# Kernel optimization log

Measured on AMD Instinct MI355X. Metric: run time of the kernel, lower is better.

## Reference

```python
import jax, jax.numpy as jnp
import numpy as np

N_NODES = 10000
DEG = 32
N_EDGES = N_NODES * DEG
IN_FEATS = 256
HEADS = 8
OUT_FEATS = 64
NEG_SLOPE = 0.2


def setup_inputs() -> dict:
    key = jax.random.key(0)
    k1, k2, k3, k4, k5 = jax.random.split(key, 5)
    feat = jax.random.normal(k1, (N_NODES, IN_FEATS), dtype=jnp.float32)
    # fc weight [in_feats, heads*out_feats] (applied as feat @ W)
    W = jax.random.normal(k2, (IN_FEATS, HEADS * OUT_FEATS), dtype=jnp.float32) * (1.0 / np.sqrt(IN_FEATS))
    attn_l = jax.random.normal(k3, (HEADS, OUT_FEATS), dtype=jnp.float32) * 0.1
    attn_r = jax.random.normal(k4, (HEADS, OUT_FEATS), dtype=jnp.float32) * 0.1
    # every node gets DEG incoming edges -> no zero in-degree (softmax well-defined)
    dst = jnp.repeat(jnp.arange(N_NODES, dtype=jnp.int32), DEG)
    src = jax.random.randint(k5, (N_EDGES,), 0, N_NODES, dtype=jnp.int32)
    return {"feat": feat, "W": W, "attn_l": attn_l, "attn_r": attn_r, "src": src, "dst": dst}


def reference(feat, W, attn_l, attn_r, src, dst):
    N = feat.shape[0]
    H, D = attn_l.shape
    # linear projection: [N, H, D]
    ft = (feat @ W).reshape(N, H, D)
    # per-node additive attention logits: [N, H]
    el = jnp.einsum('nhd,hd->nh', ft, attn_l)
    er = jnp.einsum('nhd,hd->nh', ft, attn_r)
    # edge logits (u_add_v) + LeakyReLU: [E, H]
    e = el[src] + er[dst]
    e = jnp.where(e > 0, e, NEG_SLOPE * e)
    # edge softmax segmented by destination node
    m = jax.ops.segment_max(e, dst, num_segments=N)          # [N, H]
    ex = jnp.exp(e - m[dst])                                  # [E, H]
    denom = jax.ops.segment_sum(ex, dst, num_segments=N)     # [N, H]
    a = ex / denom[dst]                                       # [E, H]
    # weighted aggregation (u_mul_e -> sum): [N, H, D]
    rst = jax.ops.segment_sum(ft[src] * a[:, :, None], dst, num_segments=N)
    # module returns attention with trailing singleton dim ([E, H, 1])
    return rst, a[:, :, None]
```

## Files before the change

kernel.cpp:

```cpp
#include <hip/hip_runtime.h>

#define N_NODES   10000
#define M_PAD     10112
#define DEG       32
#define IN_FEATS  256
#define HEADS     8
#define OUT_FEATS 64
#define HD        512
#define NEG_SLOPE 0.2f

typedef short bf16x8 __attribute__((ext_vector_type(8)));
typedef float f32x4  __attribute__((ext_vector_type(4)));

__device__ __forceinline__ ushort f2bf(float x) {
    union { float f; unsigned u; } c; c.f = x;
    unsigned r = (c.u + 0x7fffu + ((c.u >> 16) & 1u)) >> 16;
    return (ushort)r;
}
__device__ __forceinline__ float bfbits2f(unsigned hi_bits) {
    union { unsigned u; float f; } c; c.u = hi_bits;
    return c.f;
}

__global__ __launch_bounds__(256) void convert_all(const float* __restrict__ f,
                                                   ushort* __restrict__ fb,
                                                   const float* __restrict__ W,
                                                   ushort* __restrict__ Bt) {
    __shared__ ushort s[64][72];
    const int b = blockIdx.x;
    const int t = threadIdx.x;
    if (b < 2500) {
        const int i = b * 256 + t;
        const float4 v = reinterpret_cast<const float4*>(f)[i];
        ushort4 o;
        o.x = f2bf(v.x); o.y = f2bf(v.y); o.z = f2bf(v.z); o.w = f2bf(v.w);
        reinterpret_cast<ushort4*>(fb)[i] = o;
        return;
    }
    const int bb = b - 2500;
    const int kb = (bb & 3) * 64;
    const int nb = (bb >> 2) * 64;
    #pragma unroll
    for (int rep = 0; rep < 4; ++rep) {
        const int kk = rep * 16 + (t >> 4);
        const int nn = (t & 15) * 4;
        const float4 v = *reinterpret_cast<const float4*>(&W[(size_t)(kb + kk) * HD + nb + nn]);
        s[nn + 0][kk] = f2bf(v.x);
        s[nn + 1][kk] = f2bf(v.y);
        s[nn + 2][kk] = f2bf(v.z);
        s[nn + 3][kk] = f2bf(v.w);
    }
    __syncthreads();
    const int nn = t >> 2;
    const int k0 = (t & 3) * 16;
    #pragma unroll
    for (int c = 0; c < 2; ++c) {
        *reinterpret_cast<uint4*>(&Bt[(size_t)(nb + nn) * IN_FEATS + kb + k0 + c * 8]) =
            *reinterpret_cast<const uint4*>(&s[nn][k0 + c * 8]);
    }
}

__global__ __launch_bounds__(256) void gemm_logits(const ushort* __restrict__ A,
                                                   const ushort* __restrict__ Bt,
                                                   const float* __restrict__ attn_l,
                                                   const float* __restrict__ attn_r,
                                                   ushort* __restrict__ C,
                                                   float* __restrict__ el,
                                                   float* __restrict__ er) {
    __shared__ ushort As[128 * 32];
    __shared__ ushort Bs[128 * 32];
    const int t    = threadIdx.x;
    const int lane = t & 63;
    const int m0   = blockIdx.x * 128;
    const int n0   = blockIdx.y * 128;
    const int wave = t >> 6;
    const int wr   = (wave >> 1) * 64;
    const int wc   = (wave & 1) * 64;

    const int srow0 = t >> 2;
    const int srow1 = 64 + (t >> 2);
    const int sq    = t & 3;
    const int sq0   = sq ^ ((srow0 >> 1) & 3);
    const int sq1   = sq ^ ((srow1 >> 1) & 3);

    uint4 ra0, ra1, rb0, rb1;
#define LOADREGS(K0)                                                                   \
    do {                                                                               \
        ra0 = *reinterpret_cast<const uint4*>(A  + (size_t)(m0 + srow0) * IN_FEATS + (K0) + sq * 8); \
        ra1 = *reinterpret_cast<const uint4*>(A  + (size_t)(m0 + srow1) * IN_FEATS + (K0) + sq * 8); \
        rb0 = *reinterpret_cast<const uint4*>(Bt + (size_t)(n0 + srow0) * IN_FEATS + (K0) + sq * 8); \
        rb1 = *reinterpret_cast<const uint4*>(Bt + (size_t)(n0 + srow1) * IN_FEATS + (K0) + sq * 8); \
    } while (0)

    f32x4 acc[4][4];
    #pragma unroll
    for (int i = 0; i < 4; ++i)
        #pragma unroll
        for (int j = 0; j < 4; ++j)
            acc[i][j] = (f32x4){0.f, 0.f, 0.f, 0.f};

    const int rqoff = (((lane >> 4) ^ (((lane & 15) >> 1) & 3)) * 8);
    const int rl    = lane & 15;

    LOADREGS(0);
    for (int k0 = 0; k0 < IN_FEATS; k0 += 32) {
        __syncthreads();
        *reinterpret_cast<uint4*>(As + srow0 * 32 + sq0 * 8) = ra0;
        *reinterpret_cast<uint4*>(As + srow1 * 32 + sq1 * 8) = ra1;
        *reinterpret_cast<uint4*>(Bs + srow0 * 32 + sq0 * 8) = rb0;
        *reinterpret_cast<uint4*>(Bs + srow1 * 32 + sq1 * 8) = rb1;
        __syncthreads();
        if (k0 + 32 < IN_FEATS) LOADREGS(k0 + 32);

        bf16x8 af[4], bfr[4];
        #pragma unroll
        for (int i = 0; i < 4; ++i)
            af[i] = *reinterpret_cast<const bf16x8*>(As + (wr + i * 16 + rl) * 32 + rqoff);
        #pragma unroll
        for (int j = 0; j < 4; ++j)
            bfr[j] = *reinterpret_cast<const bf16x8*>(Bs + (wc + j * 16 + rl) * 32 + rqoff);
        #pragma unroll
        for (int i = 0; i < 4; ++i)
            #pragma unroll
            for (int j = 0; j < 4; ++j)
                acc[i][j] = __builtin_amdgcn_mfma_f32_16x16x32_bf16(af[i], bfr[j], acc[i][j], 0, 0, 0);
    }
#undef LOADREGS

    const int g    = lane >> 4;
    const int hblk = (n0 + wc) >> 6;
    float al[4], ar[4];
    #pragma unroll
    for (int j = 0; j < 4; ++j) {
        al[j] = attn_l[hblk * OUT_FEATS + j * 16 + rl];
        ar[j] = attn_r[hblk * OUT_FEATS + j * 16 + rl];
    }

    #pragma unroll
    for (int i = 0; i < 4; ++i) {
        #pragma unroll
        for (int r = 0; r < 4; ++r) {
            const int gm = m0 + wr + i * 16 + g * 4 + r;
            ushort* dst = C + (size_t)gm * HD + n0 + wc + rl;
            float sl = 0.f, sr = 0.f;
            #pragma unroll
            for (int j = 0; j < 4; ++j) {
                dst[j * 16] = f2bf(acc[i][j][r]);
                sl = fmaf(acc[i][j][r], al[j], sl);
                sr = fmaf(acc[i][j][r], ar[j], sr);
            }
            sl += __shfl_xor(sl, 1, 64); sr += __shfl_xor(sr, 1, 64);
            sl += __shfl_xor(sl, 2, 64); sr += __shfl_xor(sr, 2, 64);
            sl += __shfl_xor(sl, 4, 64); sr += __shfl_xor(sr, 4, 64);
            sl += __shfl_xor(sl, 8, 64); sr += __shfl_xor(sr, 8, 64);
            if (rl == 0 && gm < N_NODES) {
                el[gm * HEADS + hblk] = sl;
                er[gm * HEADS + hblk] = sr;
            }
        }
    }
}

__global__ __launch_bounds__(256) void softmax_kernel(const float* __restrict__ el,
                                                      const float* __restrict__ er,
                                                      const int* __restrict__ src,
                                                      float* __restrict__ out_a) {
    __shared__ int   s_src[DEG];
    __shared__ float s_a[DEG][HEADS];

    const int n = blockIdx.x;
    const int t = threadIdx.x;

    if (t < DEG) s_src[t] = src[n * DEG + t];
    __syncthreads();

    const int h = t >> 5;
    const int j = t & 31;
    const int s = s_src[j];
    float e = el[s * HEADS + h] + er[n * HEADS + h];
    e = (e > 0.f) ? e : NEG_SLOPE * e;

    float m = e;
    #pragma unroll
    for (int msk = 16; msk; msk >>= 1) m = fmaxf(m, __shfl_xor(m, msk, 64));
    const float ex = __expf(e - m);
    float sum = ex;
    #pragma unroll
    for (int msk = 16; msk; msk >>= 1) sum += __shfl_xor(sum, msk, 64);
    s_a[j][h] = ex / sum;
    __syncthreads();

    out_a[(size_t)n * 256 + t] = s_a[t >> 3][t & 7];
}

__global__ __launch_bounds__(256) void agg_static(const uint* __restrict__ ftb_dw,
                                                  const float* __restrict__ el,
                                                  const float* __restrict__ er,
                                                  const int* __restrict__ src,
                                                  float* __restrict__ rst) {
    __shared__ int   s_src[8][DEG];
    __shared__ float s_a[8][DEG];

    const int b = blockIdx.x;
    const int s = b & 7;
    const int c = b >> 3;
    const int t = threadIdx.x;
    const int w  = t >> 6;
    const int l  = t & 63;
    const int hi = l >> 5;
    const int li = l & 31;
    const int wn = 2 * w + hi;

    s_src[t >> 5][t & 31] = src[c * 256 + t];

    const int n     = c * 8 + wn;
    const int dwcol = s * 32 + li;

    uint uv[DEG];
    #pragma unroll
    for (int j = 0; j < DEG; ++j)
        uv[j] = ftb_dw[(size_t)s_src[wn][j] * 256 + dwcol];

    float e = el[s_src[wn][li] * HEADS + s] + er[n * HEADS + s];
    e = (e > 0.f) ? e : NEG_SLOPE * e;
    float m = e;
    #pragma unroll
    for (int msk = 16; msk; msk >>= 1) m = fmaxf(m, __shfl_xor(m, msk, 64));
    const float ex = __expf(e - m);
    float sum = ex;
    #pragma unroll
    for (int msk = 16; msk; msk >>= 1) sum += __shfl_xor(sum, msk, 64);
    s_a[wn][li] = ex / sum;

    float a0 = 0.f, a1 = 0.f;
    #pragma unroll
    for (int j = 0; j < DEG; ++j) {
        const float wt = s_a[wn][j];
        a0 = fmaf(wt, bfbits2f(uv[j] << 16), a0);
        a1 = fmaf(wt, bfbits2f(uv[j] & 0xffff0000u), a1);
    }
    *reinterpret_cast<float2*>(&rst[(size_t)n * HD + s * 64 + 2 * li]) = make_float2(a0, a1);
}

extern "C" void kernel_launch(void* const* d_in, const int* in_sizes, int n_in,
                              void* d_out, int out_size, void* d_ws, size_t ws_size,
                              hipStream_t stream) {
    const float* feat   = (const float*)d_in[0];
    const float* W      = (const float*)d_in[1];
    const float* attn_l = (const float*)d_in[2];
    const float* attn_r = (const float*)d_in[3];
    const int*   src    = (const int*)d_in[4];

    float* out_rst = (float*)d_out;
    float* out_a   = out_rst + (size_t)N_NODES * HD;

    char* w = (char*)d_ws;
    ushort* feat_bf = (ushort*)w;  w += (size_t)M_PAD * IN_FEATS * 2;
    ushort* W_bt    = (ushort*)w;  w += (size_t)HD * IN_FEATS * 2;
    ushort* ftb     = (ushort*)w;  w += (size_t)M_PAD * HD * 2;
    float*  el      = (float*)w;   w += (size_t)N_NODES * HEADS * 4;
    float*  er      = (float*)w;   w += (size_t)N_NODES * HEADS * 4;

    convert_all<<<2532, 256, 0, stream>>>(feat, feat_bf, W, W_bt);
    gemm_logits<<<dim3(M_PAD / 128, HD / 128), 256, 0, stream>>>(feat_bf, W_bt, attn_l, attn_r,
                                                                 ftb, el, er);
    softmax_kernel<<<N_NODES, 256, 0, stream>>>(el, er, src, out_a);
    agg_static<<<N_NODES / 8 * 8, 256, 0, stream>>>((const uint*)ftb, el, er, src, out_rst);
}
```

Measured before the change: 60.97 us.

## Fuse feat bf16 conversion into GEMM loads and reuse softmax weights in aggregation

The GEMM now reads fp32 features directly, converts them to bf16 in registers before staging to LDS, and guards out-of-range rows. This removes the separate feature conversion pass and its intermediate buffer. The softmax kernel also writes a head-major copy of the attention weights, which the aggregation kernel loads instead of recomputing logits, max and exp. The trade-off is double the A-operand global traffic in the GEMM, plus an extra 10 MB write and read of attention weights.

Result: slower. 79.81 us (+30.9%).

```diff
diff --git a/kernel.cpp b/kernel.cpp
--- a/kernel.cpp
+++ b/kernel.cpp
@@ -17,29 +17,21 @@
     unsigned r = (c.u + 0x7fffu + ((c.u >> 16) & 1u)) >> 16;
     return (ushort)r;
 }
+__device__ __forceinline__ uint pack2(float lo, float hi) {
+    return (uint)f2bf(lo) | ((uint)f2bf(hi) << 16);
+}
 __device__ __forceinline__ float bfbits2f(unsigned hi_bits) {
     union { unsigned u; float f; } c; c.u = hi_bits;
     return c.f;
 }
 
-__global__ __launch_bounds__(256) void convert_all(const float* __restrict__ f,
-                                                   ushort* __restrict__ fb,
-                                                   const float* __restrict__ W,
-                                                   ushort* __restrict__ Bt) {
+__global__ __launch_bounds__(256) void convert_W(const float* __restrict__ W,
+                                                 ushort* __restrict__ Bt) {
     __shared__ ushort s[64][72];
-    const int b = blockIdx.x;
-    const int t = threadIdx.x;
-    if (b < 2500) {
-        const int i = b * 256 + t;
-        const float4 v = reinterpret_cast<const float4*>(f)[i];
-        ushort4 o;
-        o.x = f2bf(v.x); o.y = f2bf(v.y); o.z = f2bf(v.z); o.w = f2bf(v.w);
-        reinterpret_cast<ushort4*>(fb)[i] = o;
-        return;
-    }
-    const int bb = b - 2500;
+    const int bb = blockIdx.x;
     const int kb = (bb & 3) * 64;
     const int nb = (bb >> 2) * 64;
+    const int t  = threadIdx.x;
     #pragma unroll
     for (int rep = 0; rep < 4; ++rep) {
         const int kk = rep * 16 + (t >> 4);
@@ -60,7 +52,7 @@
     }
 }
 
-__global__ __launch_bounds__(256) void gemm_logits(const ushort* __restrict__ A,
+__global__ __launch_bounds__(256) void gemm_logits(const float* __restrict__ A,
                                                    const ushort* __restrict__ Bt,
                                                    const float* __restrict__ attn_l,
                                                    const float* __restrict__ attn_r,
@@ -82,14 +74,20 @@
     const int sq    = t & 3;
     const int sq0   = sq ^ ((srow0 >> 1) & 3);
     const int sq1   = sq ^ ((srow1 >> 1) & 3);
-
-    uint4 ra0, ra1, rb0, rb1;
-#define LOADREGS(K0)                                                                   \
-    do {                                                                               \
-        ra0 = *reinterpret_cast<const uint4*>(A  + (size_t)(m0 + srow0) * IN_FEATS + (K0) + sq * 8); \
-        ra1 = *reinterpret_cast<const uint4*>(A  + (size_t)(m0 + srow1) * IN_FEATS + (K0) + sq * 8); \
-        rb0 = *reinterpret_cast<const uint4*>(Bt + (size_t)(n0 + srow0) * IN_FEATS + (K0) + sq * 8); \
-        rb1 = *reinterpret_cast<const uint4*>(Bt + (size_t)(n0 + srow1) * IN_FEATS + (K0) + sq * 8); \
+    const int gm0   = m0 + srow0;
+    const int gm1   = m0 + srow1;
+
+    float4 fa0a, fa0b, fa1a, fa1b;
+    uint4  rb0, rb1;
+    const float4 z4 = make_float4(0.f, 0.f, 0.f, 0.f);
+#define LOADREGS(K0)                                                                       \
+    do {                                                                                   \
+        fa0a = (gm0 < N_NODES) ? *reinterpret_cast<const float4*>(A + (size_t)gm0 * IN_FEATS + (K0) + sq * 8)     : z4; \
+        fa0b = (gm0 < N_NODES) ? *reinterpret_cast<const float4*>(A + (size_t)gm0 * IN_FEATS + (K0) + sq * 8 + 4) : z4; \
+        fa1a = (gm1 < N_NODES) ? *reinterpret_cast<const float4*>(A + (size_t)gm1 * IN_FEATS + (K0) + sq * 8)     : z4; \
+        fa1b = (gm1 < N_NODES) ? *reinterpret_cast<const float4*>(A + (size_t)gm1 * IN_FEATS + (K0) + sq * 8 + 4) : z4; \
+        rb0  = *reinterpret_cast<const uint4*>(Bt + (size_t)(n0 + srow0) * IN_FEATS + (K0) + sq * 8);             \
+        rb1  = *reinterpret_cast<const uint4*>(Bt + (size_t)(n0 + srow1) * IN_FEATS + (K0) + sq * 8);             \
     } while (0)
 
     f32x4 acc[4][4];
@@ -105,10 +103,16 @@
     LOADREGS(0);
     for (int k0 = 0; k0 < IN_FEATS; k0 += 32) {
         __syncthreads();
-        *reinterpret_cast<uint4*>(As + srow0 * 32 + sq0 * 8) = ra0;
-        *reinterpret_cast<uint4*>(As + srow1 * 32 + sq1 * 8) = ra1;
-        *reinterpret_cast<uint4*>(Bs + srow0 * 32 + sq0 * 8) = rb0;
-        *reinterpret_cast<uint4*>(Bs + srow1 * 32 + sq1 * 8) = rb1;
+        {
+            const uint4 ra0 = make_uint4(pack2(fa0a.x, fa0a.y), pack2(fa0a.z, fa0a.w),
+                                         pack2(fa0b.x, fa0b.y), pack2(fa0b.z, fa0b.w));
+            const uint4 ra1 = make_uint4(pack2(fa1a.x, fa1a.y), pack2(fa1a.z, fa1a.w),
+                                         pack2(fa1b.x, fa1b.y), pack2(fa1b.z, fa1b.w));
+            *reinterpret_cast<uint4*>(As + srow0 * 32 + sq0 * 8) = ra0;
+            *reinterpret_cast<uint4*>(As + srow1 * 32 + sq1 * 8) = ra1;
+            *reinterpret_cast<uint4*>(Bs + srow0 * 32 + sq0 * 8) = rb0;
+            *reinterpret_cast<uint4*>(Bs + srow1 * 32 + sq1 * 8) = rb1;
+        }
         __syncthreads();
         if (k0 + 32 < IN_FEATS) LOADREGS(k0 + 32);
 
@@ -164,7 +168,8 @@
 __global__ __launch_bounds__(256) void softmax_kernel(const float* __restrict__ el,
                                                       const float* __restrict__ er,
                                                       const int* __restrict__ src,
-                                                      float* __restrict__ out_a) {
+                                                      float* __restrict__ out_a,
+                                                      float* __restrict__ a_t) {
     __shared__ int   s_src[DEG];
     __shared__ float s_a[DEG][HEADS];
 
@@ -191,46 +196,36 @@
     __syncthreads();
 
     out_a[(size_t)n * 256 + t] = s_a[t >> 3][t & 7];
-}
-
-__global__ __launch_bounds__(256) void agg_static(const uint* __restrict__ ftb_dw,
-                                                  const float* __restrict__ el,
-                                                  const float* __restrict__ er,
-                                                  const int* __restrict__ src,
-                                                  float* __restrict__ rst) {
+    a_t[(size_t)n * 256 + t]   = s_a[t & 31][t >> 5];
+}
+
+__global__ __launch_bounds__(256) void agg_slice(const uint* __restrict__ ftb_dw,
+                                                 const float* __restrict__ a_t,
+                                                 const int* __restrict__ src,
+                                                 float* __restrict__ rst) {
     __shared__ int   s_src[8][DEG];
     __shared__ float s_a[8][DEG];
 
-    const int b = blockIdx.x;
-    const int s = b & 7;
-    const int c = b >> 3;
-    const int t = threadIdx.x;
+    const int b  = blockIdx.x;
+    const int s  = b & 7;
+    const int c  = b >> 3;
+    const int t  = threadIdx.x;
     const int w  = t >> 6;
     const int l  = t & 63;
     const int hi = l >> 5;
     const int li = l & 31;
     const int wn = 2 * w + hi;
-
-    s_src[t >> 5][t & 31] = src[c * 256 + t];
-
-    const int n     = c * 8 + wn;
+    const int n  = c * 8 + wn;
+
+    s_src[wn][li] = src[n * DEG + li];
+    s_a[wn][li]   = a_t[(size_t)n * 256 + s * 32 + li];
+
     const int dwcol = s * 32 + li;
 
     uint uv[DEG];
     #pragma unroll
     for (int j = 0; j < DEG; ++j)
         uv[j] = ftb_dw[(size_t)s_src[wn][j] * 256 + dwcol];
-
-    float e = el[s_src[wn][li] * HEADS + s] + er[n * HEADS + s];
-    e = (e > 0.f) ? e : NEG_SLOPE * e;
-    float m = e;
-    #pragma unroll
-    for (int msk = 16; msk; msk >>= 1) m = fmaxf(m, __shfl_xor(m, msk, 64));
-    const float ex = __expf(e - m);
-    float sum = ex;
-    #pragma unroll
-    for (int msk = 16; msk; msk >>= 1) sum += __shfl_xor(sum, msk, 64);
-    s_a[wn][li] = ex / sum;
 
     float a0 = 0.f, a1 = 0.f;
     #pragma unroll
@@ -255,15 +250,15 @@
     float* out_a   = out_rst + (size_t)N_NODES * HD;
 
     char* w = (char*)d_ws;
-    ushort* feat_bf = (ushort*)w;  w += (size_t)M_PAD * IN_FEATS * 2;
-    ushort* W_bt    = (ushort*)w;  w += (size_t)HD * IN_FEATS * 2;
-    ushort* ftb     = (ushort*)w;  w += (size_t)M_PAD * HD * 2;
-    float*  el      = (float*)w;   w += (size_t)N_NODES * HEADS * 4;
-    float*  er      = (float*)w;   w += (size_t)N_NODES * HEADS * 4;
-
-    convert_all<<<2532, 256, 0, stream>>>(feat, feat_bf, W, W_bt);
-    gemm_logits<<<dim3(M_PAD / 128, HD / 128), 256, 0, stream>>>(feat_bf, W_bt, attn_l, attn_r,
+    ushort* W_bt = (ushort*)w;  w += (size_t)HD * IN_FEATS * 2;
+    ushort* ftb  = (ushort*)w;  w += (size_t)M_PAD * HD * 2;
+    float*  el   = (float*)w;   w += (size_t)N_NODES * HEADS * 4;
+    float*  er   = (float*)w;   w += (size_t)N_NODES * HEADS * 4;
+    float*  a_t  = (float*)w;   w += (size_t)N_NODES * 256 * 4;
+
+    convert_W<<<32, 256, 0, stream>>>(W, W_bt);
+    gemm_logits<<<dim3(M_PAD / 128, HD / 128), 256, 0, stream>>>(feat, W_bt, attn_l, attn_r,
                                                                  ftb, el, er);
-    softmax_kernel<<<N_NODES, 256, 0, stream>>>(el, er, src, out_a);
-    agg_static<<<N_NODES / 8 * 8, 256, 0, stream>>>((const uint*)ftb, el, er, src, out_rst);
-}
+    softmax_kernel<<<N_NODES, 256, 0, stream>>>(el, er, src, out_a, a_t);
+    agg_slice<<<N_NODES / 8 * 8, 256, 0, stream>>>((const uint*)ftb, a_t, src, out_rst);
+}
```

## Shrink GEMM tiles to one head per block and reuse softmax weights in aggregation

Applied to the files above, without the earlier changes.

The projection GEMM now uses 64x64 tiles with one head per block column, which quadruples the block count. Per-wave partial logits are combined through shared memory before el/er are written. The softmax kernel also writes a head-major copy of the attention weights, which the aggregation kernel reads instead of recomputing the edge softmax. This removes the duplicated exp and shuffle work in aggregation, at the cost of an extra 10 MB workspace write and read plus a smaller per-block MFMA tile with less reuse.

Result: faster. 55.81 us, median of 2 (-8.5%).

```diff
diff --git a/kernel.cpp b/kernel.cpp
--- a/kernel.cpp
+++ b/kernel.cpp
@@ -67,84 +67,83 @@
                                                    ushort* __restrict__ C,
                                                    float* __restrict__ el,
                                                    float* __restrict__ er) {
-    __shared__ ushort As[128 * 32];
-    __shared__ ushort Bs[128 * 32];
+    __shared__ ushort As[64 * 32];
+    __shared__ ushort Bs[64 * 32];
+    __shared__ float  s_l[2][64];
+    __shared__ float  s_r[2][64];
+
     const int t    = threadIdx.x;
     const int lane = t & 63;
-    const int m0   = blockIdx.x * 128;
-    const int n0   = blockIdx.y * 128;
+    const int m0   = blockIdx.x * 64;
+    const int head = blockIdx.y;
+    const int n0   = head * 64;
     const int wave = t >> 6;
-    const int wr   = (wave >> 1) * 64;
-    const int wc   = (wave & 1) * 64;
-
-    const int srow0 = t >> 2;
-    const int srow1 = 64 + (t >> 2);
-    const int sq    = t & 3;
-    const int sq0   = sq ^ ((srow0 >> 1) & 3);
-    const int sq1   = sq ^ ((srow1 >> 1) & 3);
-
-    uint4 ra0, ra1, rb0, rb1;
-#define LOADREGS(K0)                                                                   \
-    do {                                                                               \
-        ra0 = *reinterpret_cast<const uint4*>(A  + (size_t)(m0 + srow0) * IN_FEATS + (K0) + sq * 8); \
-        ra1 = *reinterpret_cast<const uint4*>(A  + (size_t)(m0 + srow1) * IN_FEATS + (K0) + sq * 8); \
-        rb0 = *reinterpret_cast<const uint4*>(Bt + (size_t)(n0 + srow0) * IN_FEATS + (K0) + sq * 8); \
-        rb1 = *reinterpret_cast<const uint4*>(Bt + (size_t)(n0 + srow1) * IN_FEATS + (K0) + sq * 8); \
+    const int wr   = (wave >> 1) * 32;
+    const int wc   = (wave & 1) * 32;
+    const int wx   = wave & 1;
+
+    const int srow = t >> 2;
+    const int sq   = t & 3;
+    const int sqs  = sq ^ ((srow >> 1) & 3);
+
+    uint4 ra, rb;
+#define LOADREGS(K0)                                                                    \
+    do {                                                                                \
+        ra = *reinterpret_cast<const uint4*>(A  + (size_t)(m0 + srow) * IN_FEATS + (K0) + sq * 8); \
+        rb = *reinterpret_cast<const uint4*>(Bt + (size_t)(n0 + srow) * IN_FEATS + (K0) + sq * 8); \
     } while (0)
 
-    f32x4 acc[4][4];
-    #pragma unroll
-    for (int i = 0; i < 4; ++i)
-        #pragma unroll
-        for (int j = 0; j < 4; ++j)
+    f32x4 acc[2][2];
+    #pragma unroll
+    for (int i = 0; i < 2; ++i)
+        #pragma unroll
+        for (int j = 0; j < 2; ++j)
             acc[i][j] = (f32x4){0.f, 0.f, 0.f, 0.f};
 
-    const int rqoff = (((lane >> 4) ^ (((lane & 15) >> 1) & 3)) * 8);
     const int rl    = lane & 15;
+    const int rqoff = (((lane >> 4) ^ ((rl >> 1) & 3)) * 8);
 
     LOADREGS(0);
     for (int k0 = 0; k0 < IN_FEATS; k0 += 32) {
         __syncthreads();
-        *reinterpret_cast<uint4*>(As + srow0 * 32 + sq0 * 8) = ra0;
-        *reinterpret_cast<uint4*>(As + srow1 * 32 + sq1 * 8) = ra1;
-        *reinterpret_cast<uint4*>(Bs + srow0 * 32 + sq0 * 8) = rb0;
-        *reinterpret_cast<uint4*>(Bs + srow1 * 32 + sq1 * 8) = rb1;
+        *reinterpret_cast<uint4*>(As + srow * 32 + sqs * 8) = ra;
+        *reinterpret_cast<uint4*>(Bs + srow * 32 + sqs * 8) = rb;
         __syncthreads();
         if (k0 + 32 < IN_FEATS) LOADREGS(k0 + 32);
 
-        bf16x8 af[4], bfr[4];
-        #pragma unroll
-        for (int i = 0; i < 4; ++i)
+        bf16x8 af[2], bfr[2];
+        #pragma unroll
+        for (int i = 0; i < 2; ++i)
             af[i] = *reinterpret_cast<const bf16x8*>(As + (wr + i * 16 + rl) * 32 + rqoff);
         #pragma unroll
-        for (int j = 0; j < 4; ++j)
+        for (int j = 0; j < 2; ++j)
             bfr[j] = *reinterpret_cast<const bf16x8*>(Bs + (wc + j * 16 + rl) * 32 + rqoff);
         #pragma unroll
-        for (int i = 0; i < 4; ++i)
+        for (int i = 0; i < 2; ++i)
             #pragma unroll
-            for (int j = 0; j < 4; ++j)
+            for (int j = 0; j < 2; ++j)
                 acc[i][j] = __builtin_amdgcn_mfma_f32_16x16x32_bf16(af[i], bfr[j], acc[i][j], 0, 0, 0);
     }
 #undef LOADREGS
 
-    const int g    = lane >> 4;
-    const int hblk = (n0 + wc) >> 6;
-    float al[4], ar[4];
-    #pragma unroll
-    for (int j = 0; j < 4; ++j) {
-        al[j] = attn_l[hblk * OUT_FEATS + j * 16 + rl];
-        ar[j] = attn_r[hblk * OUT_FEATS + j * 16 + rl];
-    }
-
-    #pragma unroll
-    for (int i = 0; i < 4; ++i) {
+    const int g = lane >> 4;
+    float al[2], ar[2];
+    #pragma unroll
+    for (int j = 0; j < 2; ++j) {
+        al[j] = attn_l[n0 + wc + j * 16 + rl];
+        ar[j] = attn_r[n0 + wc + j * 16 + rl];
+    }
+
+    #pragma unroll
+    for (int i = 0; i < 2; ++i) {
         #pragma unroll
         for (int r = 0; r < 4; ++r) {
-            const int gm = m0 + wr + i * 16 + g * 4 + r;
+            const int row = wr + i * 16 + g * 4 + r;
+            const int gm  = m0 + row;
             ushort* dst = C + (size_t)gm * HD + n0 + wc + rl;
             float sl = 0.f, sr = 0.f;
             #pragma unroll
-            for (int j = 0; j < 4; ++j) {
+            for (int j = 0; j < 2; ++j) {
                 dst[j * 16] = f2bf(acc[i][j][r]);
                 sl = fmaf(acc[i][j][r], al[j], sl);
                 sr = fmaf(acc[i][j][r], ar[j], sr);
@@ -153,10 +152,18 @@
             sl += __shfl_xor(sl, 2, 64); sr += __shfl_xor(sr, 2, 64);
             sl += __shfl_xor(sl, 4, 64); sr += __shfl_xor(sr, 4, 64);
             sl += __shfl_xor(sl, 8, 64); sr += __shfl_xor(sr, 8, 64);
-            if (rl == 0 && gm < N_NODES) {
-                el[gm * HEADS + hblk] = sl;
-                er[gm * HEADS + hblk] = sr;
+            if (rl == 0) {
+                s_l[wx][row] = sl;
+                s_r[wx][row] = sr;
             }
+        }
+    }
+    __syncthreads();
+    if (t < 64) {
+        const int gm = m0 + t;
+        if (gm < N_NODES) {
+            el[gm * HEADS + head] = s_l[0][t] + s_l[1][t];
+            er[gm * HEADS + head] = s_r[0][t] + s_r[1][t];
         }
     }
 }
@@ -164,7 +171,8 @@
 __global__ __launch_bounds__(256) void softmax_kernel(const float* __restrict__ el,
                                                       const float* __restrict__ er,
                                                       const int* __restrict__ src,
-                                                      float* __restrict__ out_a) {
+                                                      float* __restrict__ out_a,
+                                                      float* __restrict__ a_t) {
     __shared__ int   s_src[DEG];
     __shared__ float s_a[DEG][HEADS];
 
@@ -191,46 +199,36 @@
     __syncthreads();
 
     out_a[(size_t)n * 256 + t] = s_a[t >> 3][t & 7];
-}
-
-__global__ __launch_bounds__(256) void agg_static(const uint* __restrict__ ftb_dw,
-                                                  const float* __restrict__ el,
-                                                  const float* __restrict__ er,
-                                                  const int* __restrict__ src,
-                                                  float* __restrict__ rst) {
+    a_t[(size_t)n * 256 + t]   = s_a[t & 31][t >> 5];
+}
+
+__global__ __launch_bounds__(256) void agg_slice(const uint* __restrict__ ftb_dw,
+                                                 const float* __restrict__ a_t,
+                                                 const int* __restrict__ src,
+                                                 float* __restrict__ rst) {
     __shared__ int   s_src[8][DEG];
     __shared__ float s_a[8][DEG];
 
-    const int b = blockIdx.x;
-    const int s = b & 7;
-    const int c = b >> 3;
-    const int t = threadIdx.x;
+    const int b  = blockIdx.x;
+    const int s  = b & 7;
+    const int c  = b >> 3;
+    const int t  = threadIdx.x;
     const int w  = t >> 6;
     const int l  = t & 63;
     const int hi = l >> 5;
     const int li = l & 31;
     const int wn = 2 * w + hi;
-
-    s_src[t >> 5][t & 31] = src[c * 256 + t];
-
-    const int n     = c * 8 + wn;
+    const int n  = c * 8 + wn;
+
+    s_src[wn][li] = src[n * DEG + li];
+    s_a[wn][li]   = a_t[(size_t)n * 256 + s * 32 + li];
+
     const int dwcol = s * 32 + li;
 
     uint uv[DEG];
     #pragma unroll
     for (int j = 0; j < DEG; ++j)
         uv[j] = ftb_dw[(size_t)s_src[wn][j] * 256 + dwcol];
-
-    float e = el[s_src[wn][li] * HEADS + s] + er[n * HEADS + s];
-    e = (e > 0.f) ? e : NEG_SLOPE * e;
-    float m = e;
-    #pragma unroll
-    for (int msk = 16; msk; msk >>= 1) m = fmaxf(m, __shfl_xor(m, msk, 64));
-    const float ex = __expf(e - m);
-    float sum = ex;
-    #pragma unroll
-    for (int msk = 16; msk; msk >>= 1) sum += __shfl_xor(sum, msk, 64);
-    s_a[wn][li] = ex / sum;
 
     float a0 = 0.f, a1 = 0.f;
     #pragma unroll
@@ -260,10 +258,11 @@
     ushort* ftb     = (ushort*)w;  w += (size_t)M_PAD * HD * 2;
     float*  el      = (float*)w;   w += (size_t)N_NODES * HEADS * 4;
     float*  er      = (float*)w;   w += (size_t)N_NODES * HEADS * 4;
+    float*  a_t     = (float*)w;   w += (size_t)N_NODES * 256 * 4;
 
     convert_all<<<2532, 256, 0, stream>>>(feat, feat_bf, W, W_bt);
-    gemm_logits<<<dim3(M_PAD / 128, HD / 128), 256, 0, stream>>>(feat_bf, W_bt, attn_l, attn_r,
-                                                                 ftb, el, er);
-    softmax_kernel<<<N_NODES, 256, 0, stream>>>(el, er, src, out_a);
-    agg_static<<<N_NODES / 8 * 8, 256, 0, stream>>>((const uint*)ftb, el, er, src, out_rst);
-}
+    gemm_logits<<<dim3(M_PAD / 64, HEADS), 256, 0, stream>>>(feat_bf, W_bt, attn_l, attn_r,
+                                                             ftb, el, er);
+    softmax_kernel<<<N_NODES, 256, 0, stream>>>(el, er, src, out_a, a_t);
+    agg_slice<<<N_NODES / 8 * 8, 256, 0, stream>>>((const uint*)ftb, a_t, src, out_rst);
+}
```
